# Kernel tuning notes

Hardware: AMD Instinct MI355X
Metric: run time of the kernel (lower is better)

Reference implementation:

```python
import jax, jax.numpy as jnp
import numpy as np

B, F, D, V = 8192, 26, 32, 100000
H1, H2 = 128, 128  # cin_size
U1, U2 = 400, 400  # dnn hidden units


def setup_inputs() -> dict:
    key = jax.random.key(0)
    ks = jax.random.split(key, 12)
    s = 0.05  # keep activations/sigmoid in a sane range
    return {
        "dense_inputs": jax.random.normal(ks[0], (B, 13), jnp.float32),
        "sparse_inputs": jax.random.randint(ks[1], (B, F), 0, V, jnp.int32),
        "E": jax.random.normal(ks[2], (F, V, D), jnp.float32) * s,
        "W_cin0": jax.random.normal(ks[3], (F, F, H1), jnp.float32) * s,
        "W_cin1": jax.random.normal(ks[4], (F, H1, H2), jnp.float32) * s,
        "W1": jax.random.normal(ks[5], (F * D, U1), jnp.float32) * s,
        "b1": jnp.zeros((U1,), jnp.float32),
        "W2": jax.random.normal(ks[6], (U1, U2), jnp.float32) * s,
        "b2": jnp.zeros((U2,), jnp.float32),
        "w_lin": jax.random.normal(ks[7], (F, 1), jnp.float32) * s,
        "b_lin": jnp.zeros((1,), jnp.float32),
        "w_out": jax.random.normal(ks[8], (1 + H1 + H2 + U2 + 13, 1), jnp.float32) * s,
        "b_out": jnp.zeros((1,), jnp.float32),
    }


def reference(dense_inputs, sparse_inputs, E, W_cin0, W_cin1, W1, b1, W2, b2,
              w_lin, b_lin, w_out, b_out):
    # Linear part: Dense(1) applied to raw (cast) sparse ids, as in the TF code.
    linear_out = sparse_inputs.astype(jnp.float32) @ w_lin + b_lin  # [B,1]

    # Embedding lookup: per-field tables. embed[b,f,:] = E[f, sparse[b,f], :]
    embed = E[jnp.arange(F)[None, :], sparse_inputs]  # [B,F,D]

    # CIN. The split->matmul->reshape->conv1d chain is exactly:
    #   x_{k+1}[b,h,d] = sum_{i,j} W_k[i,j,h] * X0[b,i,d] * x_k[b,j,d]
    X0 = embed
    x1 = jnp.einsum('bid,bjd,ijh->bhd', X0, X0, W_cin0)   # [B,H1,D]
    x2 = jnp.einsum('bid,bjd,ijh->bhd', X0, x1, W_cin1)   # [B,H2,D]
    cin_out = jnp.concatenate([x1, x2], axis=1).sum(axis=-1)  # [B,H1+H2]

    # DNN on flattened embeddings (dropout rate 0 -> identity at inference).
    v = embed.reshape(B, F * D)
    h = jax.nn.relu(v @ W1 + b1)
    h = jax.nn.relu(h @ W2 + b2)  # [B,U2]

    total = jnp.concatenate([linear_out, cin_out, h, dense_inputs], axis=-1)
    return jax.nn.sigmoid(total @ w_out + b_out)  # [B,1]
```

## Files before the change

kernel.cpp:

```cpp
#include <hip/hip_runtime.h>
#include <hip/hip_bf16.h>
#include <math.h>

typedef __attribute__((ext_vector_type(8))) short bf16x8;
typedef __attribute__((ext_vector_type(4))) float f32x4;

#define B_ 8192
#define F_ 26
#define D_ 32
#define V_ 100000
#define NP_ 351
#define KP_ 352

static const size_t OFF_VB   = 0;
static const size_t OFF_FD0  = 13631488;
static const size_t OFF_PDC2 = 13664256;
static const size_t OFF_PDH2 = 13795328;
static const size_t OFF_G    = 13926400;
static const size_t OFF_H1B  = 68452352;
static const size_t OFF_W0T  = 75005952;
static const size_t OFF_WC1T = 75096064;
static const size_t OFF_W1T  = 75948032;
static const size_t OFF_W2T  = 76613632;

static __device__ __forceinline__ unsigned short f2b(float f) {
    unsigned int u = __float_as_uint(f);
    return (unsigned short)((u + 0x7FFF + ((u >> 16) & 1)) >> 16);
}
static __device__ __forceinline__ unsigned short f2bt(float f) {
    return (unsigned short)(__float_as_uint(f) >> 16);
}
static __device__ __forceinline__ unsigned int pk2t(float a, float b) {
    return __builtin_amdgcn_perm(__float_as_uint(b), __float_as_uint(a), 0x07060302u);
}
static __device__ __forceinline__ float bf2f(unsigned short u) {
    return __uint_as_float(((unsigned int)u) << 16);
}

static __device__ __forceinline__ void transpose_body(
    const float* __restrict__ src, unsigned short* __restrict__ dst,
    int K, int N, int bx, int by)
{
    __shared__ float tl[32][33];
    const int lx = threadIdx.x & 31, ly = threadIdx.x >> 5;
    const int n0 = bx * 32, k0 = by * 32;
#pragma unroll
    for (int i = 0; i < 4; ++i) {
        int k = k0 + ly + i * 8, n = n0 + lx;
        if (k < K && n < N) tl[ly + i * 8][lx] = src[(size_t)k * N + n];
    }
    __syncthreads();
#pragma unroll
    for (int i = 0; i < 4; ++i) {
        int n = n0 + ly + i * 8, k = k0 + lx;
        if (k < K && n < N) dst[(size_t)n * K + k] = f2b(tl[lx][ly + i * 8]);
    }
}

__global__ __launch_bounds__(256) void k0_all(
    const float* __restrict__ W0, const float* __restrict__ Wc1,
    const float* __restrict__ W1, const float* __restrict__ W2,
    unsigned short* __restrict__ W0t, unsigned short* __restrict__ Wc1t,
    unsigned short* __restrict__ W1t, unsigned short* __restrict__ W2t)
{
    int bid = blockIdx.x;
    if (bid < 176) {
        int g = bid * 256 + threadIdx.x;
        if (g < 128 * KP_) {
            int h = g / KP_, p = g % KP_;
            float w = 0.f;
            if (p < NP_) {
                int i = 0, base = 0;
                while (base + (F_ - i) <= p) { base += F_ - i; ++i; }
                int j = i + (p - base);
                w = W0[(i * F_ + j) * 128 + h];
                if (i != j) w += W0[(j * F_ + i) * 128 + h];
            }
            W0t[g] = f2b(w);
        }
        return;
    }
    bid -= 176;
    const float* src; unsigned short* dst; int K, N, nx;
    if (bid < 416)               { src = Wc1; dst = Wc1t; K = 3328; N = 128; nx = 4; }
    else if ((bid -= 416) < 338) { src = W1;  dst = W1t;  K = 832;  N = 400; nx = 13; }
    else                         { bid -= 338; src = W2; dst = W2t; K = 400; N = 400; nx = 13; }
    transpose_body(src, dst, K, N, bid % nx, bid / nx);
}

__global__ __launch_bounds__(256) void k1_embed_cin(
    const int*   __restrict__ sparse,
    const float* __restrict__ E,
    const unsigned short* __restrict__ W0t,
    const float* __restrict__ wlin,
    const float* __restrict__ blin,
    const float* __restrict__ wout,
    unsigned short* __restrict__ vb,
    float* __restrict__ fdot0,
    unsigned short* __restrict__ G)
{
    __shared__ __align__(16) unsigned short embB[64][40];
    __shared__ __align__(16) unsigned short Pbuf[64 * 360];
    __shared__ float wdot[4];
    __shared__ float linv[52];
    __shared__ int   idxs[52];
    __shared__ unsigned char pI[NP_], pJ[NP_];

    const int b0 = blockIdx.x * 2, t = threadIdx.x;

    if (t < 52) {
        int bb = t >= 26 ? 1 : 0, ff = t - bb * 26;
        int id = sparse[(b0 + bb) * F_ + ff];
        idxs[t] = id;
        linv[t] = (float)id * wlin[ff];
    }
    if (t < F_) {
        int i = t, base = F_ * i - (i * (i - 1)) / 2;
        for (int j = i; j < F_; ++j) { pI[base + j - i] = (unsigned char)i; pJ[base + j - i] = (unsigned char)j; }
    }
    __syncthreads();

    for (int r = t; r < 416; r += 256) {
        int f = r >> 3, q = r & 7;
        int bb = f >= 26 ? 1 : 0, ff = f - bb * 26;
        float4 v4 = *(const float4*)(E + ((size_t)ff * V_ + idxs[f]) * D_ + q * 4);
        uint2 uu; uu.x = pk2t(v4.x, v4.y); uu.y = pk2t(v4.z, v4.w);
        *(uint2*)&embB[bb * 32 + ff][q * 4] = uu;
        *(uint2*)(vb + (size_t)(b0 + bb) * 832 + ff * 32 + q * 4) = uu;
    }
    if (t < 192) {
        int row = t >> 4, bb = row >= 6 ? 1 : 0, rr = row - bb * 6;
        *(unsigned int*)&embB[bb * 32 + 26 + rr][(t & 15) * 2] = 0u;
    }
    __syncthreads();

    {
        const int d = t & 31, sub = t >> 5;
        const int bb = sub & 1, pb = sub >> 1;
        const int e0 = bb * 32;
        const int p0 = pb * 88;
        unsigned short* Prow = &Pbuf[(e0 + d) * 360];
        for (int k = 0; k < 44; ++k) {
            int p = p0 + 2 * k;
            float a = bf2f(embB[e0 + pI[p]][d]) * bf2f(embB[e0 + pJ[p]][d]);
            float c = (p + 1 < NP_) ? bf2f(embB[e0 + pI[p + 1]][d]) * bf2f(embB[e0 + pJ[p + 1]][d]) : 0.f;
            *(unsigned int*)&Prow[p] = pk2t(a, c);
        }
    }
    __syncthreads();

    const int wave = t >> 6, lane = t & 63;
    const int lr = lane & 15, lg = lane >> 4;
    const int bb = wave & 1;
    const int h0 = (wave >> 1) * 64;
    f32x4 acc[2][4] = {};
    {
        const unsigned short* Ab = &Pbuf[(bb * 32 + lr) * 360];
        const unsigned short* Bb = W0t + (size_t)(h0 + lr) * KP_ + lg * 8;
        for (int kt = 0; kt < 11; ++kt) {
            const int ko = kt * 32 + lg * 8;
            bf16x8 a0 = *(const bf16x8*)(Ab + ko);
            bf16x8 a1 = *(const bf16x8*)(Ab + 16 * 360 + ko);
#pragma unroll
            for (int n = 0; n < 4; ++n) {
                bf16x8 bw = *(const bf16x8*)(Bb + (size_t)(n * 16) * KP_ + kt * 32);
                acc[0][n] = __builtin_amdgcn_mfma_f32_16x16x32_bf16(a0, bw, acc[0][n], 0, 0, 0);
                acc[1][n] = __builtin_amdgcn_mfma_f32_16x16x32_bf16(a1, bw, acc[1][n], 0, 0, 0);
            }
        }
    }

    float dotv = 0.f;
#pragma unroll
    for (int n = 0; n < 4; ++n) {
        float s = acc[0][n][0] + acc[0][n][1] + acc[0][n][2] + acc[0][n][3]
                + acc[1][n][0] + acc[1][n][1] + acc[1][n][2] + acc[1][n][3];
        s += __shfl_xor(s, 16, 64);
        s += __shfl_xor(s, 32, 64);
        if (lg == 0) dotv += s * wout[1 + h0 + n * 16 + lr];
    }
#pragma unroll
    for (int off = 1; off <= 32; off <<= 1) dotv += __shfl_xor(dotv, off, 64);
    if (lane == 0) wdot[wave] = dotv;
    __syncthreads();

#pragma unroll
    for (int n = 0; n < 4; ++n) {
        const int base = ((bb << 7) + h0 + n * 16 + lr) * 40;
#pragma unroll
        for (int mi = 0; mi < 2; ++mi) {
            *(unsigned int*)&Pbuf[base + mi * 16 + lg * 4]     = pk2t(acc[mi][n][0], acc[mi][n][1]);
            *(unsigned int*)&Pbuf[base + mi * 16 + lg * 4 + 2] = pk2t(acc[mi][n][2], acc[mi][n][3]);
        }
    }
    __syncthreads();

    if (t < 2) {
        float s = blin[0];
        for (int f = 0; f < F_; ++f) s += linv[t * 26 + f];
        fdot0[b0 + t] = s * wout[0] + wdot[t] + wdot[t + 2];
    }

    {
        bf16x8 ga0 = *(const bf16x8*)&embB[bb * 32 + lr][lg * 8];
        bf16x8 ga1 = *(const bf16x8*)&embB[bb * 32 + 16 + lr][lg * 8];
        unsigned short* Gb = G + (size_t)(b0 + bb) * 3328;
#pragma unroll
        for (int n = 0; n < 4; ++n) {
            const int j = h0 + n * 16 + lr;
            bf16x8 xb = *(const bf16x8*)&Pbuf[((bb << 7) + j) * 40 + lg * 8];
            f32x4 g0 = {}, g1 = {};
            g0 = __builtin_amdgcn_mfma_f32_16x16x32_bf16(ga0, xb, g0, 0, 0, 0);
            g1 = __builtin_amdgcn_mfma_f32_16x16x32_bf16(ga1, xb, g1, 0, 0, 0);
#pragma unroll
            for (int r = 0; r < 4; ++r) {
                int i0 = lg * 4 + r;
                Gb[i0 * 128 + j] = f2bt(g0[r]);
                int i1 = 16 + lg * 4 + r;
                if (i1 < F_) Gb[i1 * 128 + j] = f2bt(g1[r]);
            }
        }
    }
}

static __device__ __forceinline__ void gemm_core(
    const unsigned short* __restrict__ A, int lda,
    const unsigned short* __restrict__ Bt, int ldb, int N,
    int m0, int n0, int kbase, int kend,
    unsigned short (*As)[40], unsigned short (*Bs)[40],
    f32x4 (*acc)[2])
{
    const int t = threadIdx.x;
    const int wave = t >> 6, lane = t & 63;
    const int lr = lane & 15, lg = lane >> 4;
    const int wn = wave * 32;
    const int ar = t >> 2, kg = (t & 3) * 8;

    const unsigned short* aptr = A  + (size_t)(m0 + ar) * lda + kbase + kg;
    const unsigned short* bp0  = Bt + (size_t)(n0 + ar) * ldb + kbase + kg;
    const unsigned short* bp1  = Bt + (size_t)(n0 + 64 + ar) * ldb + kbase + kg;
    const bool bn0 = (n0 + ar) < N, bn1 = (n0 + 64 + ar) < N;
    const uint4 z4 = make_uint4(0u, 0u, 0u, 0u);
    const int nkt = (kend - kbase + 31) >> 5;
    uint4 av, bv0, bv1;
    {
        int k = kbase + kg;
        av  = (k < kend)        ? *(const uint4*)aptr : z4;
        bv0 = (bn0 && k < kend) ? *(const uint4*)bp0  : z4;
        bv1 = (bn1 && k < kend) ? *(const uint4*)bp1  : z4;
    }
    for (int kt = 0; kt < nkt; ++kt) {
        *(uint4*)&As[ar][kg]      = av;
        *(uint4*)&Bs[ar][kg]      = bv0;
        *(uint4*)&Bs[64 + ar][kg] = bv1;
        __syncthreads();
        if (kt + 1 < nkt) {
            int kn = kbase + (kt + 1) * 32 + kg;
            av  = (kn < kend)        ? *(const uint4*)(aptr + (kt + 1) * 32) : z4;
            bv0 = (bn0 && kn < kend) ? *(const uint4*)(bp0  + (kt + 1) * 32) : z4;
            bv1 = (bn1 && kn < kend) ? *(const uint4*)(bp1  + (kt + 1) * 32) : z4;
        }
        bf16x8 af[4], bfr[2];
#pragma unroll
        for (int i = 0; i < 4; ++i) af[i]  = *(const bf16x8*)&As[i * 16 + lr][lg * 8];
#pragma unroll
        for (int j = 0; j < 2; ++j) bfr[j] = *(const bf16x8*)&Bs[wn + j * 16 + lr][lg * 8];
#pragma unroll
        for (int i = 0; i < 4; ++i)
#pragma unroll
            for (int j = 0; j < 2; ++j)
                acc[i][j] = __builtin_amdgcn_mfma_f32_16x16x32_bf16(af[i], bfr[j], acc[i][j], 0, 0, 0);
        __syncthreads();
    }
}

__global__ __launch_bounds__(256) void k2_h1_cin2(
    const unsigned short* __restrict__ vb, const unsigned short* __restrict__ W1t,
    const float* __restrict__ b1, unsigned short* __restrict__ h1b,
    const unsigned short* __restrict__ G, const unsigned short* __restrict__ Wc1t,
    const float* __restrict__ wout, float* __restrict__ pdc2)
{
    __shared__ __align__(16) unsigned short As[64][40];
    __shared__ __align__(16) unsigned short Bs[128][40];
    __shared__ float red[4][64];
    const int t = threadIdx.x;
    const int wave = t >> 6, lane = t & 63;
    const int lr = lane & 15, lg = lane >> 4;
    const int m0 = blockIdx.y * 64;
    f32x4 acc[4][2] = {};

    if (blockIdx.z == 0) {
        const int n0 = blockIdx.x * 128;
        gemm_core(vb, 832, W1t, 832, 400, m0, n0, 0, 832, As, Bs, acc);
#pragma unroll
        for (int i = 0; i < 4; ++i) {
            int mrow = m0 + i * 16 + lg * 4;
#pragma unroll
            for (int j = 0; j < 2; ++j) {
                int col = n0 + wave * 32 + j * 16 + lr;
                if (col >= 400) continue;
                float bb = b1[col];
#pragma unroll
                for (int r = 0; r < 4; ++r)
                    h1b[(size_t)(mrow + r) * 400 + col] = f2bt(fmaxf(acc[i][j][r] + bb, 0.f));
            }
        }
    } else {
        const int chunk = blockIdx.x;
        gemm_core(G, 3328, Wc1t, 3328, 128, m0, 0, chunk * 832, chunk * 832 + 832, As, Bs, acc);
        float v[4][4];
#pragma unroll
        for (int i = 0; i < 4; ++i)
#pragma unroll
            for (int r = 0; r < 4; ++r) {
                float s = 0.f;
#pragma unroll
                for (int j = 0; j < 2; ++j)
                    s = fmaf(acc[i][j][r], wout[129 + wave * 32 + j * 16 + lr], s);
#pragma unroll
                for (int off = 1; off <= 8; off <<= 1) s += __shfl_xor(s, off, 64);
                v[i][r] = s;
            }
        if (lr == 0) {
#pragma unroll
            for (int i = 0; i < 4; ++i)
#pragma unroll
                for (int r = 0; r < 4; ++r) red[wave][i * 16 + lg * 4 + r] = v[i][r];
        }
        __syncthreads();
        if (t < 64) pdc2[(size_t)chunk * B_ + m0 + t] = red[0][t] + red[1][t] + red[2][t] + red[3][t];
    }
}

__global__ __launch_bounds__(256) void k2_h2(
    const unsigned short* __restrict__ h1b, const unsigned short* __restrict__ W2t,
    const float* __restrict__ b2, const float* __restrict__ wout,
    float* __restrict__ pdh2)
{
    __shared__ __align__(16) unsigned short As[64][40];
    __shared__ __align__(16) unsigned short Bs[128][40];
    __shared__ float red[4][64];
    const int t = threadIdx.x;
    const int wave = t >> 6, lane = t & 63;
    const int lr = lane & 15, lg = lane >> 4;
    const int m0 = blockIdx.y * 64, n0 = blockIdx.x * 128;
    f32x4 acc[4][2] = {};
    gemm_core(h1b, 400, W2t, 400, 400, m0, n0, 0, 400, As, Bs, acc);
    float v[4][4];
#pragma unroll
    for (int i = 0; i < 4; ++i)
#pragma unroll
        for (int r = 0; r < 4; ++r) {
            float s = 0.f;
#pragma unroll
            for (int j = 0; j < 2; ++j) {
                int col = n0 + wave * 32 + j * 16 + lr;
                if (col < 400)
                    s = fmaf(fmaxf(acc[i][j][r] + b2[col], 0.f), wout[257 + col], s);
            }
#pragma unroll
            for (int off = 1; off <= 8; off <<= 1) s += __shfl_xor(s, off, 64);
            v[i][r] = s;
        }
    if (lr == 0) {
#pragma unroll
        for (int i = 0; i < 4; ++i)
#pragma unroll
            for (int r = 0; r < 4; ++r) red[wave][i * 16 + lg * 4 + r] = v[i][r];
    }
    __syncthreads();
    if (t < 64) pdh2[(size_t)blockIdx.x * B_ + m0 + t] = red[0][t] + red[1][t] + red[2][t] + red[3][t];
}

__global__ __launch_bounds__(256) void k3_final(
    const float* __restrict__ fdot0,
    const float* __restrict__ pdc2,
    const float* __restrict__ pdh2,
    const float* __restrict__ dense,
    const float* __restrict__ wout,
    const float* __restrict__ bout,
    float* __restrict__ out)
{
    const int b = blockIdx.x * 256 + threadIdx.x;
    float s = fdot0[b];
#pragma unroll
    for (int z = 0; z < 4; ++z) s += pdc2[(size_t)z * B_ + b];
#pragma unroll
    for (int z = 0; z < 4; ++z) s += pdh2[(size_t)z * B_ + b];
#pragma unroll
    for (int q = 0; q < 13; ++q) s = fmaf(dense[(size_t)b * 13 + q], wout[657 + q], s);
    out[b] = 1.f / (1.f + expf(-(s + bout[0])));
}

extern "C" void kernel_launch(void* const* d_in, const int* in_sizes, int n_in,
                              void* d_out, int out_size, void* d_ws, size_t ws_size,
                              hipStream_t stream) {
    const float* dense  = (const float*)d_in[0];
    const int*   sparse = (const int*)  d_in[1];
    const float* E      = (const float*)d_in[2];
    const float* W0     = (const float*)d_in[3];
    const float* Wc1    = (const float*)d_in[4];
    const float* W1     = (const float*)d_in[5];
    const float* b1     = (const float*)d_in[6];
    const float* W2     = (const float*)d_in[7];
    const float* b2     = (const float*)d_in[8];
    const float* wlin   = (const float*)d_in[9];
    const float* blin   = (const float*)d_in[10];
    const float* wout   = (const float*)d_in[11];
    const float* bout   = (const float*)d_in[12];
    float* out = (float*)d_out;

    char* ws = (char*)d_ws;
    unsigned short* vb    = (unsigned short*)(ws + OFF_VB);
    float*          fdot0 = (float*)(ws + OFF_FD0);
    float*          pdc2  = (float*)(ws + OFF_PDC2);
    float*          pdh2  = (float*)(ws + OFF_PDH2);
    unsigned short* G     = (unsigned short*)(ws + OFF_G);
    unsigned short* h1b   = (unsigned short*)(ws + OFF_H1B);
    unsigned short* W0t   = (unsigned short*)(ws + OFF_W0T);
    unsigned short* Wc1t  = (unsigned short*)(ws + OFF_WC1T);
    unsigned short* W1t   = (unsigned short*)(ws + OFF_W1T);
    unsigned short* W2t   = (unsigned short*)(ws + OFF_W2T);

    k0_all<<<176 + 416 + 338 + 169, 256, 0, stream>>>(W0, Wc1, W1, W2, W0t, Wc1t, W1t, W2t);
    k1_embed_cin<<<B_ / 2, 256, 0, stream>>>(sparse, E, W0t, wlin, blin, wout, vb, fdot0, G);
    k2_h1_cin2<<<dim3(4, 128, 2), 256, 0, stream>>>(vb, W1t, b1, h1b, G, Wc1t, wout, pdc2);
    k2_h2<<<dim3(4, 128), 256, 0, stream>>>(h1b, W2t, b2, wout, pdh2);
    k3_final<<<B_ / 256, 256, 0, stream>>>(fdot0, pdc2, pdh2, dense, wout, bout, out);
}
```

Baseline: 534.9 us.

## Fold CIN layer-2 weights with output weights to eliminate G tensor and GEMM

Because only the sum over d of x2 dotted with w_out is needed, the CIN layer-2 weights are pre-contracted with the output weights into a small F×128 matrix. k1 then folds the per-sample G tile directly into a scalar, so the large bf16 G intermediate (~54 MB write plus read) and the 3328-deep GEMM half of k2 go away. It adds a small precompute in k0 and an extra reduction in k1, and changes the rounding order of that term.

```diff
diff --git a/kernel.cpp b/kernel.cpp
--- a/kernel.cpp
+++ b/kernel.cpp
@@ -14,14 +14,12 @@
 
 static const size_t OFF_VB   = 0;
 static const size_t OFF_FD0  = 13631488;
-static const size_t OFF_PDC2 = 13664256;
-static const size_t OFF_PDH2 = 13795328;
-static const size_t OFF_G    = 13926400;
-static const size_t OFF_H1B  = 68452352;
-static const size_t OFF_W0T  = 75005952;
-static const size_t OFF_WC1T = 75096064;
-static const size_t OFF_W1T  = 75948032;
-static const size_t OFF_W2T  = 76613632;
+static const size_t OFF_PDH2 = 13664256;
+static const size_t OFF_H1B  = 13795328;
+static const size_t OFF_W0T  = 20348928;
+static const size_t OFF_W1T  = 20439040;
+static const size_t OFF_W2T  = 21104640;
+static const size_t OFF_MWT  = 21424640;
 
 static __device__ __forceinline__ unsigned short f2b(float f) {
     unsigned int u = __float_as_uint(f);
@@ -60,8 +58,9 @@
 __global__ __launch_bounds__(256) void k0_all(
     const float* __restrict__ W0, const float* __restrict__ Wc1,
     const float* __restrict__ W1, const float* __restrict__ W2,
-    unsigned short* __restrict__ W0t, unsigned short* __restrict__ Wc1t,
-    unsigned short* __restrict__ W1t, unsigned short* __restrict__ W2t)
+    const float* __restrict__ wout,
+    unsigned short* __restrict__ W0t, unsigned short* __restrict__ W1t,
+    unsigned short* __restrict__ W2t, float* __restrict__ Mwt)
 {
     int bid = blockIdx.x;
     if (bid < 176) {
@@ -81,11 +80,22 @@
         return;
     }
     bid -= 176;
-    const float* src; unsigned short* dst; int K, N, nx;
-    if (bid < 416)               { src = Wc1; dst = Wc1t; K = 3328; N = 128; nx = 4; }
-    else if ((bid -= 416) < 338) { src = W1;  dst = W1t;  K = 832;  N = 400; nx = 13; }
-    else                         { bid -= 338; src = W2; dst = W2t; K = 400; N = 400; nx = 13; }
-    transpose_body(src, dst, K, N, bid % nx, bid / nx);
+    if (bid < 338) { transpose_body(W1, W1t, 832, 400, bid % 13, bid / 13); return; }
+    bid -= 338;
+    if (bid < 169) { transpose_body(W2, W2t, 400, 400, bid % 13, bid / 13); return; }
+    bid -= 169;
+    {
+        int g = bid * 256 + threadIdx.x;
+        if (g < 128 * 32) {
+            int j = g >> 5, i = g & 31;
+            float s = 0.f;
+            if (i < F_) {
+                const float* row = Wc1 + ((size_t)i * 128 + j) * 128;
+                for (int h = 0; h < 128; ++h) s = fmaf(row[h], wout[129 + h], s);
+            }
+            Mwt[g] = s;
+        }
+    }
 }
 
 __global__ __launch_bounds__(256) void k1_embed_cin(
@@ -95,9 +105,9 @@
     const float* __restrict__ wlin,
     const float* __restrict__ blin,
     const float* __restrict__ wout,
+    const float* __restrict__ Mwt,
     unsigned short* __restrict__ vb,
-    float* __restrict__ fdot0,
-    unsigned short* __restrict__ G)
+    float* __restrict__ fdot0)
 {
     __shared__ __align__(16) unsigned short embB[64][40];
     __shared__ __align__(16) unsigned short Pbuf[64 * 360];
@@ -179,9 +189,6 @@
         s += __shfl_xor(s, 32, 64);
         if (lg == 0) dotv += s * wout[1 + h0 + n * 16 + lr];
     }
-#pragma unroll
-    for (int off = 1; off <= 32; off <<= 1) dotv += __shfl_xor(dotv, off, 64);
-    if (lane == 0) wdot[wave] = dotv;
     __syncthreads();
 
 #pragma unroll
@@ -195,16 +202,9 @@
     }
     __syncthreads();
 
-    if (t < 2) {
-        float s = blin[0];
-        for (int f = 0; f < F_; ++f) s += linv[t * 26 + f];
-        fdot0[b0 + t] = s * wout[0] + wdot[t] + wdot[t + 2];
-    }
-
     {
         bf16x8 ga0 = *(const bf16x8*)&embB[bb * 32 + lr][lg * 8];
         bf16x8 ga1 = *(const bf16x8*)&embB[bb * 32 + 16 + lr][lg * 8];
-        unsigned short* Gb = G + (size_t)(b0 + bb) * 3328;
 #pragma unroll
         for (int n = 0; n < 4; ++n) {
             const int j = h0 + n * 16 + lr;
@@ -212,14 +212,22 @@
             f32x4 g0 = {}, g1 = {};
             g0 = __builtin_amdgcn_mfma_f32_16x16x32_bf16(ga0, xb, g0, 0, 0, 0);
             g1 = __builtin_amdgcn_mfma_f32_16x16x32_bf16(ga1, xb, g1, 0, 0, 0);
-#pragma unroll
-            for (int r = 0; r < 4; ++r) {
-                int i0 = lg * 4 + r;
-                Gb[i0 * 128 + j] = f2bt(g0[r]);
-                int i1 = 16 + lg * 4 + r;
-                if (i1 < F_) Gb[i1 * 128 + j] = f2bt(g1[r]);
-            }
-        }
+            const float* mr = Mwt + j * 32;
+            float4 m0 = *(const float4*)(mr + lg * 4);
+            float4 m1 = *(const float4*)(mr + 16 + lg * 4);
+            dotv += g0[0] * m0.x + g0[1] * m0.y + g0[2] * m0.z + g0[3] * m0.w
+                  + g1[0] * m1.x + g1[1] * m1.y + g1[2] * m1.z + g1[3] * m1.w;
+        }
+    }
+#pragma unroll
+    for (int off = 1; off <= 32; off <<= 1) dotv += __shfl_xor(dotv, off, 64);
+    if (lane == 0) wdot[wave] = dotv;
+    __syncthreads();
+
+    if (t < 2) {
+        float s = blin[0];
+        for (int f = 0; f < F_; ++f) s += linv[t * 26 + f];
+        fdot0[b0 + t] = s * wout[0] + wdot[t] + wdot[t + 2];
     }
 }
 
@@ -274,61 +282,30 @@
     }
 }
 
-__global__ __launch_bounds__(256) void k2_h1_cin2(
+__global__ __launch_bounds__(256) void k2_h1(
     const unsigned short* __restrict__ vb, const unsigned short* __restrict__ W1t,
-    const float* __restrict__ b1, unsigned short* __restrict__ h1b,
-    const unsigned short* __restrict__ G, const unsigned short* __restrict__ Wc1t,
-    const float* __restrict__ wout, float* __restrict__ pdc2)
+    const float* __restrict__ b1, unsigned short* __restrict__ h1b)
 {
     __shared__ __align__(16) unsigned short As[64][40];
     __shared__ __align__(16) unsigned short Bs[128][40];
-    __shared__ float red[4][64];
     const int t = threadIdx.x;
     const int wave = t >> 6, lane = t & 63;
     const int lr = lane & 15, lg = lane >> 4;
-    const int m0 = blockIdx.y * 64;
+    const int m0 = blockIdx.y * 64, n0 = blockIdx.x * 128;
     f32x4 acc[4][2] = {};
-
-    if (blockIdx.z == 0) {
-        const int n0 = blockIdx.x * 128;
-        gemm_core(vb, 832, W1t, 832, 400, m0, n0, 0, 832, As, Bs, acc);
-#pragma unroll
-        for (int i = 0; i < 4; ++i) {
-            int mrow = m0 + i * 16 + lg * 4;
-#pragma unroll
-            for (int j = 0; j < 2; ++j) {
-                int col = n0 + wave * 32 + j * 16 + lr;
-                if (col >= 400) continue;
-                float bb = b1[col];
-#pragma unroll
-                for (int r = 0; r < 4; ++r)
-                    h1b[(size_t)(mrow + r) * 400 + col] = f2bt(fmaxf(acc[i][j][r] + bb, 0.f));
-            }
-        }
-    } else {
-        const int chunk = blockIdx.x;
-        gemm_core(G, 3328, Wc1t, 3328, 128, m0, 0, chunk * 832, chunk * 832 + 832, As, Bs, acc);
-        float v[4][4];
-#pragma unroll
-        for (int i = 0; i < 4; ++i)
-#pragma unroll
-            for (int r = 0; r < 4; ++r) {
-                float s = 0.f;
-#pragma unroll
-                for (int j = 0; j < 2; ++j)
-                    s = fmaf(acc[i][j][r], wout[129 + wave * 32 + j * 16 + lr], s);
-#pragma unroll
-                for (int off = 1; off <= 8; off <<= 1) s += __shfl_xor(s, off, 64);
-                v[i][r] = s;
-            }
-        if (lr == 0) {
-#pragma unroll
-            for (int i = 0; i < 4; ++i)
-#pragma unroll
-                for (int r = 0; r < 4; ++r) red[wave][i * 16 + lg * 4 + r] = v[i][r];
-        }
-        __syncthreads();
-        if (t < 64) pdc2[(size_t)chunk * B_ + m0 + t] = red[0][t] + red[1][t] + red[2][t] + red[3][t];
+    gemm_core(vb, 832, W1t, 832, 400, m0, n0, 0, 832, As, Bs, acc);
+#pragma unroll
+    for (int i = 0; i < 4; ++i) {
+        int mrow = m0 + i * 16 + lg * 4;
+#pragma unroll
+        for (int j = 0; j < 2; ++j) {
+            int col = n0 + wave * 32 + j * 16 + lr;
+            if (col >= 400) continue;
+            float bb = b1[col];
+#pragma unroll
+            for (int r = 0; r < 4; ++r)
+                h1b[(size_t)(mrow + r) * 400 + col] = f2bt(fmaxf(acc[i][j][r] + bb, 0.f));
+        }
     }
 }
 
@@ -374,7 +351,6 @@
 
 __global__ __launch_bounds__(256) void k3_final(
     const float* __restrict__ fdot0,
-    const float* __restrict__ pdc2,
     const float* __restrict__ pdh2,
     const float* __restrict__ dense,
     const float* __restrict__ wout,
@@ -383,8 +359,6 @@
 {
     const int b = blockIdx.x * 256 + threadIdx.x;
     float s = fdot0[b];
-#pragma unroll
-    for (int z = 0; z < 4; ++z) s += pdc2[(size_t)z * B_ + b];
 #pragma unroll
     for (int z = 0; z < 4; ++z) s += pdh2[(size_t)z * B_ + b];
 #pragma unroll
@@ -413,18 +387,16 @@
     char* ws = (char*)d_ws;
     unsigned short* vb    = (unsigned short*)(ws + OFF_VB);
     float*          fdot0 = (float*)(ws + OFF_FD0);
-    float*          pdc2  = (float*)(ws + OFF_PDC2);
     float*          pdh2  = (float*)(ws + OFF_PDH2);
-    unsigned short* G     = (unsigned short*)(ws + OFF_G);
     unsigned short* h1b   = (unsigned short*)(ws + OFF_H1B);
     unsigned short* W0t   = (unsigned short*)(ws + OFF_W0T);
-    unsigned short* Wc1t  = (unsigned short*)(ws + OFF_WC1T);
     unsigned short* W1t   = (unsigned short*)(ws + OFF_W1T);
     unsigned short* W2t   = (unsigned short*)(ws + OFF_W2T);
-
-    k0_all<<<176 + 416 + 338 + 169, 256, 0, stream>>>(W0, Wc1, W1, W2, W0t, Wc1t, W1t, W2t);
-    k1_embed_cin<<<B_ / 2, 256, 0, stream>>>(sparse, E, W0t, wlin, blin, wout, vb, fdot0, G);
-    k2_h1_cin2<<<dim3(4, 128, 2), 256, 0, stream>>>(vb, W1t, b1, h1b, G, Wc1t, wout, pdc2);
+    float*          Mwt   = (float*)(ws + OFF_MWT);
+
+    k0_all<<<176 + 338 + 169 + 16, 256, 0, stream>>>(W0, Wc1, W1, W2, wout, W0t, W1t, W2t, Mwt);
+    k1_embed_cin<<<B_ / 2, 256, 0, stream>>>(sparse, E, W0t, wlin, blin, wout, Mwt, vb, fdot0);
+    k2_h1<<<dim3(4, 128), 256, 0, stream>>>(vb, W1t, b1, h1b);
     k2_h2<<<dim3(4, 128), 256, 0, stream>>>(h1b, W2t, b2, wout, pdh2);
-    k3_final<<<B_ / 256, 256, 0, stream>>>(fdot0, pdc2, pdh2, dense, wout, bout, out);
-}
+    k3_final<<<B_ / 256, 256, 0, stream>>>(fdot0, pdh2, dense, wout, bout, out);
+}
```

New measurement: 526.0 us. Within noise of the previous version (-1.7%).
